# Kernel optimization log

Hardware: AMD Instinct MI355X
Metric: run time of the kernel (lower is better)

## Reference

```python
import jax, jax.numpy as jnp
import numpy as np

# ---- static dims ----
B, L, V = 8, 512, 100000
E, NERD, COREFD = 100, 20, 20          # word / ner / coref embedding dims
H, DIS, REL, HT = 128, 20, 97, 512     # hidden, dis embed, relations, n_pairs
W, N, R, C = 512, 32, 8, 256           # DNC word len, cells, read heads, ctrl hidden
IN_SIZE = E + NERD + COREFD            # 140 == H + 12 (required by final_layer)
DNC_OUT = H + 12                        # 140
CTRL_IN = IN_SIZE + R * W               # 4236
MASK_MIN, EPS, CLIP = 0.1, 1e-6, 20.0
# interface vector layout: read keys, read strengths, write key, write strength,
# erase, write vec, free gates, alloc gate, write gate, read modes,
# write mask, read masks, fwd sharpness, bwd sharpness
XI_SIZES = [R*W, R, W, 1, W, W, R, 1, 1, 3*R, W, R*W, R, R]
XI = sum(XI_SIZES)


def setup_inputs():
    key = jax.random.key(0)
    ks = iter(jax.random.split(key, 40))
    def nrm(shape, s=0.02):
        return (jax.random.normal(next(ks), shape) * s).astype(jnp.float32)
    def ri(shape, hi):
        return jax.random.randint(next(ks), shape, 0, hi)
    return dict(
        context_idxs=ri((B, L), V),
        pos=ri((B, L), L),
        context_ner=ri((B, L), 7),
        context_char_idxs=ri((B, L, 16), 262),
        context_lens=jnp.full((B,), L, dtype=jnp.int32),
        h_mapping=jax.random.uniform(next(ks), (B, HT, L), jnp.float32) / L,
        t_mapping=jax.random.uniform(next(ks), (B, HT, L), jnp.float32) / L,
        relation_mask=jnp.ones((B, HT), jnp.float32),
        dis_h_2_t=ri((B, HT), 20),
        dis_t_2_h=ri((B, HT), 20),
        word_emb=nrm((V, E), 0.1),
        entity_emb=nrm((L, COREFD), 0.1),
        ner_emb=nrm((7, NERD), 0.1),
        dis_emb=nrm((20, DIS), 0.1),
        Wih0=nrm((CTRL_IN, 4*C)), Whh0=nrm((C, 4*C)), b0=jnp.zeros((4*C,), jnp.float32),
        Wih1=nrm((C, 4*C)), Whh1=nrm((C, 4*C)), b1=jnp.zeros((4*C,), jnp.float32),
        Wih2=nrm((C, 4*C)), Whh2=nrm((C, 4*C)), b2=jnp.zeros((4*C,), jnp.float32),
        W_xi=nrm((C, XI)), b_xi=jnp.zeros((XI,), jnp.float32),
        W_out=nrm((C + R*W, DNC_OUT)), b_out=jnp.zeros((DNC_OUT,), jnp.float32),
        W_final=nrm((DNC_OUT, 2*H)), b_final=jnp.zeros((2*H,), jnp.float32),
        W_re=nrm((2*H, H)), b_re=jnp.zeros((H,), jnp.float32),
        W_bili=nrm((REL, H+DIS, H+DIS)), b_bili=jnp.zeros((REL,), jnp.float32),
    )


def _lstm(x, h, c, Wih, Whh, b):
    z = x @ Wih + h @ Whh + b
    i, f, g, o = jnp.split(z, 4, axis=-1)
    c = jax.nn.sigmoid(f) * c + jax.nn.sigmoid(i) * jnp.tanh(g)
    h = jax.nn.sigmoid(o) * jnp.tanh(c)
    return h, c


def _content(M, key_, beta, mask):
    # M [B,N,W]; key_, mask [B,h,W]; beta [B,h] -> weights [B,h,N]
    k = key_ * mask
    Mm = M[:, None] * mask[:, :, None]                 # [B,h,N,W]
    dot = jnp.einsum('bhw,bhnw->bhn', k, Mm)
    kn = jnp.linalg.norm(k, axis=-1)[..., None]
    Mn = jnp.linalg.norm(Mm, axis=-1)
    cos = dot / (kn * Mn + EPS)
    return jax.nn.softmax(beta[..., None] * cos, axis=-1)


def _sharpen(w, s):
    w = (w + EPS) ** s[..., None]
    return w / w.sum(-1, keepdims=True)


def _dnc(x, params):
    (Wih0, Whh0, b0, Wih1, Whh1, b1, Wih2, Whh2, b2, W_xi, b_xi, W_out, b_out) = params
    Bs = x.shape[0]
    eye = jnp.eye(N, dtype=x.dtype)
    splits = np.cumsum(XI_SIZES)[:-1]

    def step(carry, x_t):
        (h0, c0, h1, c1, h2, c2, M, u, wr, ww, p, Lnk, reads) = carry
        ci = jnp.concatenate([x_t, reads.reshape(Bs, R*W)], -1)
        h0, c0 = _lstm(ci, h0, c0, Wih0, Whh0, b0)
        h1, c1 = _lstm(h0, h1, c1, Wih1, Whh1, b1)
        h2, c2 = _lstm(h1, h2, c2, Wih2, Whh2, b2)
        h = jnp.clip(h2, -CLIP, CLIP)
        xi = h @ W_xi + b_xi
        (rk, rb, wk, wb, er, wv, fg, ga, gw, rm,
         wmask, rmask, sf, sb) = jnp.split(xi, splits, axis=-1)
        rk = rk.reshape(Bs, R, W)
        rb = 1 + jax.nn.softplus(rb)                    # [B,R]
        wk = wk.reshape(Bs, 1, W)
        wb = 1 + jax.nn.softplus(wb)                    # [B,1]
        er = jax.nn.sigmoid(er)                         # [B,W]
        fg = jax.nn.sigmoid(fg)                         # [B,R]
        ga = jax.nn.sigmoid(ga)
        gw = jax.nn.sigmoid(gw)
        pi = jax.nn.softmax(rm.reshape(Bs, R, 3), -1)
        wmask = MASK_MIN + (1 - MASK_MIN) * jax.nn.sigmoid(wmask)
        rmask = MASK_MIN + (1 - MASK_MIN) * jax.nn.sigmoid(rmask).reshape(Bs, R, W)
        sf = 1 + jax.nn.softplus(sf)
        sb = 1 + jax.nn.softplus(sb)

        # retention / usage
        psi = jnp.prod(1 - fg[:, :, None] * wr, axis=1)  # [B,N]
        u = (u + ww - u * ww) * psi
        # allocation weighting via sorted free list
        order = jnp.argsort(u, axis=-1)
        us = jnp.take_along_axis(u, order, -1)
        cp = jnp.cumprod(jnp.concatenate([jnp.ones((Bs, 1), u.dtype), us[:, :-1]], -1), -1)
        a_s = (1 - us) * cp
        a = jnp.zeros_like(u).at[jnp.arange(Bs)[:, None], order].set(a_s)
        # write addressing (masked content + allocation)
        cw = _content(M, wk, wb, wmask[:, None, :])[:, 0]
        ww = gw * (ga * a + (1 - ga) * cw)
        # de-allocate content of freed cells, then write
        M = M * psi[:, :, None]
        M = M * (1 - ww[:, :, None] * er[:, None, :]) + ww[:, :, None] * wv[:, None, :]
        # temporal link matrix (uses previous precedence p)
        Lnk = (1 - ww[:, :, None] - ww[:, None, :]) * Lnk + ww[:, :, None] * p[:, None, :]
        Lnk = Lnk * (1 - eye)
        p = (1 - ww.sum(-1, keepdims=True)) * p + ww
        # read addressing with link sharpness control
        fw = _sharpen(jnp.einsum('bij,brj->bri', Lnk, wr), sf)
        bw = _sharpen(jnp.einsum('bji,brj->bri', Lnk, wr), sb)
        cr = _content(M, rk, rb, rmask)
        wr = pi[..., 0:1] * bw + pi[..., 1:2] * cr + pi[..., 2:3] * fw
        reads = jnp.einsum('brn,bnw->brw', wr, M)
        y = jnp.concatenate([h, reads.reshape(Bs, R*W)], -1) @ W_out + b_out
        return (h0, c0, h1, c1, h2, c2, M, u, wr, ww, p, Lnk, reads), y

    z = jnp.zeros
    carry0 = (z((Bs, C)), z((Bs, C)), z((Bs, C)), z((Bs, C)), z((Bs, C)), z((Bs, C)),
              z((Bs, N, W)), z((Bs, N)), z((Bs, R, N)), z((Bs, N)), z((Bs, N)),
              z((Bs, N, N)), z((Bs, R, W)))
    _, ys = jax.lax.scan(step, carry0, x.transpose(1, 0, 2))
    return ys.transpose(1, 0, 2)  # [B,L,DNC_OUT]


def reference(context_idxs, pos, context_ner, context_char_idxs, context_lens,
              h_mapping, t_mapping, relation_mask, dis_h_2_t, dis_t_2_h,
              word_emb, entity_emb, ner_emb, dis_emb,
              Wih0, Whh0, b0, Wih1, Whh1, b1, Wih2, Whh2, b2,
              W_xi, b_xi, W_out, b_out, W_final, b_final, W_re, b_re,
              W_bili, b_bili):
    sent = jnp.concatenate([word_emb[context_idxs], entity_emb[pos],
                            ner_emb[context_ner]], -1)      # [B,L,140]
    dnc_params = (Wih0, Whh0, b0, Wih1, Whh1, b1, Wih2, Whh2, b2,
                  W_xi, b_xi, W_out, b_out)
    out = _dnc(sent, dnc_params)                             # [B,L,140]
    out = out @ W_final + b_final                            # LockedDropout: identity (eval)
    ctx = jax.nn.relu(out @ W_re + b_re)                     # [B,L,H]
    s0 = jnp.einsum('bpl,blh->bph', h_mapping, ctx)
    t0 = jnp.einsum('bpl,blh->bph', t_mapping, ctx)
    s_rep = jnp.concatenate([s0, dis_emb[dis_h_2_t]], -1)    # [B,P,148]
    t_rep = jnp.concatenate([t0, dis_emb[dis_t_2_h]], -1)
    return jnp.einsum('bpi,kij,bpj->bpk', s_rep, W_bili, t_rep) + b_bili
```

## Files before the change

### kernel.cpp

```cpp
#include <hip/hip_runtime.h>
#include <math.h>

#define B8      8
#define LSEQ    512
#define NWG     256
#define TPB     512
#define RELK    97
#define BI      148
#define FSTR    16

#define oWA     0
#define oW1     18432
#define oW2     20480
#define oWX     22528
#define oWY     34816
#define oST     37196
#define LDSF    40948
#define LDSB    (LDSF*4)

__device__ __forceinline__ float sigf(float x){
  return (x >= 0.f) ? 1.f/(1.f + expf(-x)) : expf(x)/(1.f + expf(x));
}
__device__ __forceinline__ float spf(float x){
  return (x > 0.f) ? x + log1pf(expf(-x)) : log1pf(expf(x));
}
__device__ __forceinline__ float agld(const float* p){
  return __hip_atomic_load(p, __ATOMIC_RELAXED, __HIP_MEMORY_SCOPE_AGENT);
}
__device__ __forceinline__ void agst(float* p, float v){
  __hip_atomic_store(p, v, __ATOMIC_RELAXED, __HIP_MEMORY_SCOPE_AGENT);
}

__global__ __launch_bounds__(256)
void k_sent(const int* __restrict__ cidx, const int* __restrict__ pos,
            const int* __restrict__ ner, const float* __restrict__ wemb,
            const float* __restrict__ eemb, const float* __restrict__ nemb,
            float* __restrict__ sent)
{
  int flat = blockIdx.x*256 + threadIdx.x;
  if (flat >= B8*LSEQ*140) return;
  int d = flat % 140; int bl = flat / 140;
  float v;
  if (d < 100)      v = wemb[(size_t)cidx[bl]*100 + d];
  else if (d < 120) v = eemb[(size_t)pos[bl]*20 + (d-100)];
  else              v = nemb[(size_t)ner[bl]*20 + (d-120)];
  sent[flat] = v;
}

__global__ __launch_bounds__(256)
void k_tr(const float* __restrict__ A, const float* __restrict__ Bsrc,
          int N, int K1a, int K1b, int K2, long long total, float* __restrict__ T)
{
  long long i = (long long)blockIdx.x*256 + threadIdx.x;
  if (i >= total) return;
  int k = (int)(i % K2);
  long long c = i / K2;
  float v = 0.f;
  if (k < K1a)            v = A[(size_t)k*N + c];
  else if (k < K1a+K1b)   v = Bsrc[(size_t)(k-K1a)*N + c];
  T[i] = v;
}

__device__ __forceinline__ void gbar(int* flags, int* genrep, int seq){
  __syncthreads();
  const int tid = threadIdx.x;
  const int bid = blockIdx.x;
  if (tid == 0){
    asm volatile("s_waitcnt vmcnt(0)" ::: "memory");
    __hip_atomic_store(&flags[bid*FSTR], seq, __ATOMIC_RELAXED, __HIP_MEMORY_SCOPE_AGENT);
  }
  if (bid == 0){
    if (tid < NWG){
      while (__hip_atomic_load(&flags[tid*FSTR], __ATOMIC_RELAXED, __HIP_MEMORY_SCOPE_AGENT) < seq)
        __builtin_amdgcn_s_sleep(1);
    }
    __syncthreads();
    if (tid < NWG)
      __hip_atomic_store(&genrep[tid*FSTR], seq, __ATOMIC_RELAXED, __HIP_MEMORY_SCOPE_AGENT);
  } else if (tid == 0){
    while (__hip_atomic_load(&genrep[bid*FSTR], __ATOMIC_RELAXED, __HIP_MEMORY_SCOPE_AGENT) < seq)
      __builtin_amdgcn_s_sleep(1);
  }
  __syncthreads();
}

__device__ void mem_phase(float* lds, const float* __restrict__ xi,
                          float* __restrict__ M, float* u_g, float* ww_g,
                          float* p_g, float* wr_g, float* L_g, float* rout)
{
  const int tid = threadIdx.x;
  float* mL  = lds;
  float* mwr = lds+1024;
  float* mwrn= lds+1280;
  float* mcr = lds+1536;
  float* mfw = lds+1792;
  float* mbw = lds+2048;
  float* PSI = lds+2304;
  float* UU  = lds+2336;
  float* US  = lds+2368;
  float* AA  = lds+2400;
  float* CW  = lds+2432;
  float* WWN = lds+2464;
  float* WWO = lds+2496;
  float* PP  = lds+2528;
  int*   mord= (int*)(lds+2560);
  float* mh  = lds+2592;
  float* mpi = lds+2624;
  float* msc = lds+2648;
  float* q1  = lds+2688;
  float* q2  = lds+3200;

  if (tid < 8){
    mh[tid]    = 1.f + spf(agld(&xi[4096+tid]));
    mh[8+tid]  = 1.f + spf(agld(&xi[10283+tid]));
    mh[16+tid] = 1.f + spf(agld(&xi[10291+tid]));
    mh[24+tid] = sigf(agld(&xi[5641+tid]));
    float e0=agld(&xi[5651+3*tid]), e1=agld(&xi[5652+3*tid]), e2=agld(&xi[5653+3*tid]);
    float mx=fmaxf(e0,fmaxf(e1,e2));
    float x0=expf(e0-mx), x1=expf(e1-mx), x2=expf(e2-mx);
    float inv=1.f/(x0+x1+x2);
    mpi[tid*3]=x0*inv; mpi[tid*3+1]=x1*inv; mpi[tid*3+2]=x2*inv;
  }
  if (tid==0){ msc[0]=1.f+spf(agld(&xi[4616])); msc[1]=sigf(agld(&xi[5649])); msc[2]=sigf(agld(&xi[5650])); }
  if (tid<32){ UU[tid]=u_g[tid]; WWO[tid]=ww_g[tid]; PP[tid]=p_g[tid]; }
  if (tid<256) mwr[tid]=wr_g[tid];
  mL[tid]=L_g[tid]; mL[tid+512]=L_g[tid+512];
  { float wm = 0.1f+0.9f*sigf(agld(&xi[5675+tid])); q1[tid]=agld(&xi[4104+tid])*wm; q2[tid]=wm; }
  __syncthreads();

  if (tid<32){
    float psi=1.f;
    #pragma unroll
    for (int r=0;r<8;r++) psi *= (1.f - mh[24+r]*mwr[r*32+tid]);
    PSI[tid]=psi;
    float uo=UU[tid], wo=WWO[tid];
    UU[tid]=(uo+wo-uo*wo)*psi;
  }
  __syncthreads();
  if (tid<32){
    float un=UU[tid]; int rank=0;
    for (int m=0;m<32;m++){ float um=UU[m]; rank += (um<un)||(um==un && m<tid); }
    mord[rank]=tid;
  }
  __syncthreads();
  if (tid<32) US[tid]=UU[mord[tid]];
  __syncthreads();
  if (tid==0){ float cp=1.f; for (int j=0;j<32;j++){ AA[mord[j]]=(1.f-US[j])*cp; cp*=US[j]; } }
  __syncthreads();

  { float q=q1[tid]*q1[tid];
    for (int o=32;o;o>>=1) q += __shfl_down(q,o,64);
    if ((tid&63)==0) msc[8+(tid>>6)]=q; }
  __syncthreads();
  if (tid==0){ float q=0.f; for (int i=0;i<8;i++) q+=msc[8+i]; msc[3]=sqrtf(q); }
  __syncthreads();
  { int n=tid>>4, wsub=tid&15;
    float d=0.f,q=0.f;
    for (int i=0;i<32;i++){ int w=wsub+16*i; float m=M[(size_t)n*512+w]; float t2=m*q2[w]; d+=q1[w]*t2; q+=t2*t2; }
    for (int o=8;o;o>>=1){ d+=__shfl_down(d,o,16); q+=__shfl_down(q,o,16); }
    if (wsub==0){ float cs=d/(msc[3]*sqrtf(q)+1e-6f); CW[n]=msc[0]*cs; } }
  __syncthreads();
  if (tid==0){ float mx=-1e30f; for(int n=0;n<32;n++) mx=fmaxf(mx,CW[n]); msc[4]=mx; }
  __syncthreads();
  if (tid<32) CW[tid]=expf(CW[tid]-msc[4]);
  __syncthreads();
  if (tid==0){ float sm=0.f; for(int n=0;n<32;n++) sm+=CW[n]; msc[5]=1.f/sm; }
  __syncthreads();
  if (tid<32) CW[tid]*=msc[5];
  __syncthreads();
  if (tid<32) WWN[tid]=msc[2]*(msc[1]*AA[tid]+(1.f-msc[1])*CW[tid]);
  __syncthreads();
  { float er=sigf(agld(&xi[4617+tid])); float wv=agld(&xi[5129+tid]);
    for (int n=0;n<32;n++){ size_t idx=(size_t)n*512+tid; float m=M[idx];
      M[idx]=m*PSI[n]*(1.f-WWN[n]*er)+WWN[n]*wv; } }
  __syncthreads();
  for (int ii=0;ii<2;ii++){ int f=tid+512*ii; int i=f>>5, j=f&31;
    float nl=(1.f-WWN[i]-WWN[j])*mL[f]+WWN[i]*PP[j];
    mL[f]=(i==j)?0.f:nl; }
  __syncthreads();
  if (tid==0){ float sw=0.f; for(int n=0;n<32;n++) sw+=WWN[n]; msc[6]=sw; }
  __syncthreads();
  if (tid<32) PP[tid]=(1.f-msc[6])*PP[tid]+WWN[tid];
  __syncthreads();
  { int r=(tid>>5)&7, i=tid&31; bool isB=(tid>=256);
    float accv=0.f;
    if (!isB){ for (int j=0;j<32;j++) accv += mL[i*32+j]*mwr[r*32+j]; }
    else     { for (int j=0;j<32;j++) accv += mL[j*32+i]*mwr[r*32+j]; }
    float sp = isB? mh[16+r] : mh[8+r];
    float e = expf(sp*logf(accv+1e-6f));
    if (!isB) mfw[r*32+i]=e; else mbw[r*32+i]=e; }
  __syncthreads();
  if (tid<16){ int r=tid&7; float sm=0.f;
    if (tid<8){ for(int n=0;n<32;n++) sm+=mfw[r*32+n]; msc[16+r]=1.f/sm; }
    else      { for(int n=0;n<32;n++) sm+=mbw[r*32+n]; msc[24+r]=1.f/sm; } }
  __syncthreads();
  { int r=(tid>>5)&7, i=tid&31; bool isB=(tid>=256);
    if (!isB) mfw[r*32+i]*=msc[16+r]; else mbw[r*32+i]*=msc[24+r]; }
  __syncthreads();
  for (int r=0;r<8;r++){
    { float rm=0.1f+0.9f*sigf(agld(&xi[6187+r*512+tid]));
      q1[tid]=agld(&xi[r*512+tid])*rm; q2[tid]=rm; }
    __syncthreads();
    { float q=q1[tid]*q1[tid];
      for (int o=32;o;o>>=1) q+=__shfl_down(q,o,64);
      if ((tid&63)==0) msc[8+(tid>>6)]=q; }
    __syncthreads();
    if (tid==0){ float qq=0.f; for(int i=0;i<8;i++) qq+=msc[8+i]; msc[32]=sqrtf(qq); }
    __syncthreads();
    { int n=tid>>4, wsub=tid&15;
      float d=0.f,q=0.f;
      for (int i=0;i<32;i++){ int w=wsub+16*i; float m=M[(size_t)n*512+w]; float t2=m*q2[w]; d+=q1[w]*t2; q+=t2*t2; }
      for (int o=8;o;o>>=1){ d+=__shfl_down(d,o,16); q+=__shfl_down(q,o,16); }
      if (wsub==0){ float cs=d/(msc[32]*sqrtf(q)+1e-6f); mcr[r*32+n]=mh[r]*cs; } }
    __syncthreads();
  }
  if (tid<8){ int r=tid; float mx=-1e30f;
    for (int n=0;n<32;n++) mx=fmaxf(mx,mcr[r*32+n]);
    float sm=0.f;
    for (int n=0;n<32;n++){ float e=expf(mcr[r*32+n]-mx); mcr[r*32+n]=e; sm+=e; }
    float inv=1.f/sm;
    for (int n=0;n<32;n++) mcr[r*32+n]*=inv; }
  __syncthreads();
  if (tid<256){ int r=tid>>5, n=tid&31;
    float v=mpi[r*3]*mbw[r*32+n]+mpi[r*3+1]*mcr[r*32+n]+mpi[r*3+2]*mfw[r*32+n];
    mwrn[tid]=v; wr_g[tid]=v; }
  __syncthreads();
  { int r=tid>>6, wsub=tid&63;
    for (int i2=0;i2<8;i2++){ int w=wsub+64*i2;
      float accv=0.f;
      for (int n=0;n<32;n++) accv+=mwrn[r*32+n]*M[(size_t)n*512+w];
      agst(&rout[r*512+w], accv); } }
  if (tid<32){ u_g[tid]=UU[tid]; ww_g[tid]=WWN[tid]; p_g[tid]=PP[tid]; }
  L_g[tid]=mL[tid]; L_g[tid+512]=mL[tid+512];
}

__global__ __launch_bounds__(TPB, 1)
void dnc_persist(
  const float* __restrict__ sent,
  const float* __restrict__ Wih0, const float* __restrict__ Whh0, const float* __restrict__ b0,
  const float* __restrict__ Wih1, const float* __restrict__ Whh1, const float* __restrict__ b1,
  const float* __restrict__ Wih2, const float* __restrict__ Whh2, const float* __restrict__ b2,
  const float* __restrict__ WXIT, const float* __restrict__ bxi,
  const float* __restrict__ Wout, const float* __restrict__ bout,
  float* __restrict__ yh,
  float* __restrict__ reads,
  float* __restrict__ h0, float* __restrict__ h1,
  float* __restrict__ h2u, float* __restrict__ h2c,
  float* __restrict__ c0p, float* __restrict__ c1p, float* __restrict__ c2p,
  float* __restrict__ zp0, float* __restrict__ zp1, float* __restrict__ zp2,
  float* __restrict__ yp, float* __restrict__ xig,
  float* __restrict__ Mb, float* __restrict__ ug, float* __restrict__ wwg,
  float* __restrict__ pg, float* __restrict__ wrg, float* __restrict__ Lg,
  int* flags, int* genrep)
{
  extern __shared__ float lds[];
  const int wg  = blockIdx.x;
  const int tid = threadIdx.x;
  const int cg  = wg >> 4, kg  = wg & 15;
  const int cgB = wg >> 3, kgB = wg & 7;
  const int ycg = wg >> 6, ykg = wg & 63;
  const int xc  = tid >> 6, xk = tid & 63;
  float* stg = lds + oST;
  int seq = 0;

  for (int f=tid; f<18432; f+=TPB){
    int kk=f>>6, cc=f&63;
    int gk=kg*288+kk, gc=cg*64+cc;
    float v=0.f;
    if (gk<4236) v=Wih0[(size_t)gk*1024+gc];
    else if (gk<4492) v=Whh0[(size_t)(gk-4236)*1024+gc];
    lds[oWA+f]=v;
  }
  for (int f=tid; f<2048; f+=TPB){
    int kk=f>>5, cc=f&31;
    int gk=kgB*64+kk, gc=cgB*32+cc;
    lds[oW1+f] = (gk<256)? Wih1[(size_t)gk*1024+gc] : Whh1[(size_t)(gk-256)*1024+gc];
  }
  for (int f=tid; f<2048; f+=TPB){
    int kk=f>>5, cc=f&31;
    int gk=kgB*64+kk, gc=cgB*32+cc;
    lds[oW2+f] = (gk<256)? Wih2[(size_t)gk*1024+gc] : Whh2[(size_t)(gk-256)*1024+gc];
  }
  for (int f=tid; f<12288; f+=TPB){
    int cl=f>>8, k=f&255; int col=wg*48+cl;
    lds[oWX+f] = (col<10299)? WXIT[(size_t)col*256+k] : 0.f;
  }
  for (int f=tid; f<2380; f+=TPB){
    int kk=f/35, cc=f%35;
    int gk=ykg*68+kk, gc=ycg*35+cc;
    lds[oWY+f] = Wout[(size_t)gk*140+gc];
  }
  __syncthreads();

  #pragma unroll 1
  for (int t=0; t<LSEQ; t++){
    {
      float* sAct = stg;
      float* sActY= stg+2304;
      for (int f=tid; f<2304; f+=TPB){
        int s=f/288, kk=f%288; int g=kg*288+kk;
        float v;
        if (g<140)       v = sent[((size_t)s*512+t)*140+g];
        else if (g<4236) v = agld(&reads[s*4096+g-140]);
        else if (g<4492) v = agld(&h0[s*256+(g-4236)]);
        else             v = 0.f;
        sAct[f]=v;
      }
      if (t>0) for (int f=tid; f<544; f+=TPB){
        int s=f/68, kk=f%68; int gy=ykg*68+kk;
        sActY[f] = (gy<256)? agld(&h2c[s*256+gy]) : agld(&reads[s*4096+gy-256]);
      }
      __syncthreads();
      { int cc=tid&63, s=tid>>6;
        const float* wAl = lds+oWA;
        const float* ac  = sAct + s*288;
        float acc=0.f;
        #pragma unroll 8
        for (int kk=0; kk<288; kk++) acc += wAl[kk*64+cc]*ac[kk];
        agst(&zp0[(size_t)(kg*8+s)*1024 + cg*64+cc], acc); }
      if (t>0 && tid<280){ int s=tid/35, cc=tid%35;
        const float* wYl = lds+oWY;
        const float* ac  = sActY + s*68;
        float acc=0.f;
        #pragma unroll 4
        for (int kk=0; kk<68; kk++) acc += wYl[kk*35+cc]*ac[kk];
        agst(&yp[(size_t)(ykg*8+s)*144 + ycg*35+cc], acc); }
    }
    gbar(flags,genrep,++seq);

    if (wg < 64){
      int s = wg>>3, part = wg&7;
      float* sP = stg;
      { int j32=tid&31, q=(tid>>5)&3, kp=tid>>7;
        int col = q*256 + part*32 + j32;
        float v=0.f;
        for (int k2=kp*4; k2<kp*4+4; k2++) v += agld(&zp0[(size_t)(k2*8+s)*1024+col]);
        sP[kp*128 + q*32 + j32] = v; }
      __syncthreads();
      if (tid<32){
        int j = part*32 + tid;
        float zq[4];
        #pragma unroll
        for (int q=0;q<4;q++){ float v=0.f;
          for (int k2=0;k2<4;k2++) v += sP[k2*128+q*32+tid];
          zq[q]=v + b0[q*256+j]; }
        float cold=c0p[s*256+j];
        float cn=sigf(zq[1])*cold + sigf(zq[0])*tanhf(zq[2]);
        float h=sigf(zq[3])*tanhf(cn);
        c0p[s*256+j]=cn;
        agst(&h0[s*256+j], h);
      }
    }
    gbar(flags,genrep,++seq);

    {
      float* sAct = stg;
      for (int f=tid; f<512; f+=TPB){ int s=f>>6, kk=f&63; int g=kgB*64+kk;
        sAct[f] = (g<256)? agld(&h0[s*256+g]) : agld(&h1[s*256+g-256]); }
      __syncthreads();
      if (tid<256){ int cc=tid&31, s=tid>>5;
        const float* w1l = lds+oW1;
        const float* ac  = sAct + s*64;
        float acc=0.f;
        #pragma unroll 8
        for (int kk=0; kk<64; kk++) acc += w1l[kk*32+cc]*ac[kk];
        agst(&zp1[(size_t)(kgB*8+s)*1024 + cgB*32+cc], acc); }
    }
    gbar(flags,genrep,++seq);

    if (wg < 64){
      int s = wg>>3, part = wg&7;
      float* sP = stg;
      if (tid<256){ int j32=tid&31, q=(tid>>5)&3, kp=tid>>7;
        int col = q*256 + part*32 + j32;
        float v=0.f;
        for (int k2=kp*4; k2<kp*4+4; k2++) v += agld(&zp1[(size_t)(k2*8+s)*1024+col]);
        sP[kp*128 + q*32 + j32] = v; }
      __syncthreads();
      if (tid<32){
        int j = part*32 + tid;
        float zq[4];
        #pragma unroll
        for (int q=0;q<4;q++) zq[q]=sP[q*32+tid]+sP[128+q*32+tid]+b1[q*256+j];
        float cold=c1p[s*256+j];
        float cn=sigf(zq[1])*cold + sigf(zq[0])*tanhf(zq[2]);
        float h=sigf(zq[3])*tanhf(cn);
        c1p[s*256+j]=cn;
        agst(&h1[s*256+j], h);
      }
    }
    gbar(flags,genrep,++seq);

    {
      float* sAct = stg;
      for (int f=tid; f<512; f+=TPB){ int s=f>>6, kk=f&63; int g=kgB*64+kk;
        sAct[f] = (g<256)? agld(&h1[s*256+g]) : agld(&h2u[s*256+g-256]); }
      __syncthreads();
      if (tid<256){ int cc=tid&31, s=tid>>5;
        const float* w2l = lds+oW2;
        const float* ac  = sAct + s*64;
        float acc=0.f;
        #pragma unroll 8
        for (int kk=0; kk<64; kk++) acc += w2l[kk*32+cc]*ac[kk];
        agst(&zp2[(size_t)(kgB*8+s)*1024 + cgB*32+cc], acc); }
    }
    gbar(flags,genrep,++seq);

    if (wg < 64){
      int s = wg>>3, part = wg&7;
      float* sP = stg;
      if (tid<256){ int j32=tid&31, q=(tid>>5)&3, kp=tid>>7;
        int col = q*256 + part*32 + j32;
        float v=0.f;
        for (int k2=kp*4; k2<kp*4+4; k2++) v += agld(&zp2[(size_t)(k2*8+s)*1024+col]);
        sP[kp*128 + q*32 + j32] = v; }
      __syncthreads();
      if (tid<32){
        int j = part*32 + tid;
        float zq[4];
        #pragma unroll
        for (int q=0;q<4;q++) zq[q]=sP[q*32+tid]+sP[128+q*32+tid]+b2[q*256+j];
        float cold=c2p[s*256+j];
        float cn=sigf(zq[1])*cold + sigf(zq[0])*tanhf(zq[2]);
        float h2=sigf(zq[3])*tanhf(cn);
        float hc=fminf(fmaxf(h2,-20.f),20.f);
        c2p[s*256+j]=cn;
        agst(&h2u[s*256+j], h2);
        agst(&h2c[s*256+j], hc);
      }
    }
    gbar(flags,genrep,++seq);

    {
      float* sA2 = stg;
      for (int f=tid; f<2048; f+=TPB){ int s=f>>8, j=f&255;
        sA2[s*260+j] = agld(&h2c[s*256+j]); }
      __syncthreads();
      float accx[6][8];
      #pragma unroll
      for (int cc=0;cc<6;cc++)
        #pragma unroll
        for (int s=0;s<8;s++) accx[cc][s]=0.f;
      #pragma unroll
      for (int s=0;s<8;s++){
        float4 a = *reinterpret_cast<const float4*>(&sA2[s*260 + (xk<<2)]);
        #pragma unroll
        for (int cc=0;cc<6;cc++){
          float4 wv = *reinterpret_cast<const float4*>(&lds[oWX + (xc*6+cc)*256 + (xk<<2)]);
          accx[cc][s] += a.x*wv.x + a.y*wv.y + a.z*wv.z + a.w*wv.w;
        }
      }
      #pragma unroll
      for (int o=32;o;o>>=1)
        #pragma unroll
        for (int cc=0;cc<6;cc++)
          #pragma unroll
          for (int s=0;s<8;s++) accx[cc][s]+=__shfl_down(accx[cc][s],o,64);
      if ((tid&63)==0){
        #pragma unroll
        for (int cc=0;cc<6;cc++){
          int col = wg*48 + xc*6 + cc;
          if (col < 10299){
            #pragma unroll
            for (int s=0;s<8;s++) agst(&xig[(size_t)s*10299+col], accx[cc][s]+bxi[col]);
          }
        }
      }
    }
    gbar(flags,genrep,++seq);

    if (wg < 8){
      mem_phase(stg, xig + (size_t)wg*10299, Mb + (size_t)wg*16384,
                ug+wg*32, wwg+wg*32, pg+wg*32, wrg+wg*256, Lg+wg*1024,
                reads + wg*4096);
    } else if (wg < 148 && t > 0){
      int ty = t-1, j = wg-8;
      int s = tid>>6, kg2 = tid&63;
      float v = agld(&yp[(size_t)(kg2*8+s)*144 + j]);
      #pragma unroll
      for (int o=32;o;o>>=1) v += __shfl_down(v,o,64);
      if (kg2==0) yh[((size_t)s*512+ty)*140+j] = v + bout[j];
    }
    gbar(flags,genrep,++seq);
  }

  {
    float* sActY = stg;
    for (int f=tid; f<544; f+=TPB){
      int s=f/68, kk=f%68; int gy=ykg*68+kk;
      sActY[f] = (gy<256)? agld(&h2c[s*256+gy]) : agld(&reads[s*4096+gy-256]);
    }
    __syncthreads();
    if (tid<280){ int s=tid/35, cc=tid%35;
      const float* wYl = lds+oWY;
      const float* ac  = sActY + s*68;
      float acc=0.f;
      for (int kk=0; kk<68; kk++) acc += wYl[kk*35+cc]*ac[kk];
      agst(&yp[(size_t)(ykg*8+s)*144 + ycg*35+cc], acc); }
  }
  gbar(flags,genrep,++seq);
  if (wg>=8 && wg<148){
    int j = wg-8;
    int s = tid>>6, kg2 = tid&63;
    float v = agld(&yp[(size_t)(kg2*8+s)*144 + j]);
    #pragma unroll
    for (int o=32;o;o>>=1) v += __shfl_down(v,o,64);
    if (kg2==0) yh[((size_t)s*512+511)*140+j] = v + bout[j];
  }
}

__global__ __launch_bounds__(256)
void gemm16(int M, int N, int K,
            const float* __restrict__ A, long long sAb, int lda,
            const float* __restrict__ Bm, long long sBb, int ldb,
            float* __restrict__ C, long long sCb, int ldc,
            const float* __restrict__ bias, int relu)
{
  __shared__ float sAh[16*512];
  const int tid = threadIdx.x;
  const float* Ab = A + (size_t)blockIdx.y*sAb;
  const float* Bb = Bm + (size_t)blockIdx.y*sBb;
  float* Cb = C + (size_t)blockIdx.y*sCb;
  const int m0 = blockIdx.x*16;
  const int tot = 16*K;
  for (int f = tid; f < tot; f += 256) sAh[f] = Ab[(size_t)m0*lda + f];
  __syncthreads();
  int c = (tid & 63)*4; int rg = tid >> 6;
  if (c >= N) return;
  float acc[4][4] = {};
  for (int k=0;k<K;k++){
    float4 bv = *reinterpret_cast<const float4*>(Bb + (size_t)k*ldb + c);
    #pragma unroll
    for (int rr=0;rr<4;rr++){
      float a = sAh[(rg*4+rr)*K + k];
      acc[rr][0] += a*bv.x; acc[rr][1] += a*bv.y; acc[rr][2] += a*bv.z; acc[rr][3] += a*bv.w;
    }
  }
  for (int rr=0;rr<4;rr++){
    int m = m0 + rg*4 + rr;
    #pragma unroll
    for (int e=0;e<4;e++){
      float v = acc[rr][e] + (bias ? bias[c+e] : 0.f);
      if (relu) v = fmaxf(v, 0.f);
      Cb[(size_t)m*ldc + c + e] = v;
    }
  }
}

__global__ __launch_bounds__(256)
void bilin(const float* __restrict__ s0, const float* __restrict__ t0,
           const float* __restrict__ dis_emb, const int* __restrict__ dht,
           const int* __restrict__ dth, const float* __restrict__ Wb,
           const float* __restrict__ bb, float* __restrict__ out)
{
  __shared__ float sS[BI][33];
  __shared__ float sT[32][152];
  const int tid = threadIdx.x;
  const int bp0 = blockIdx.x*32;
  for (int f = tid; f < 32*BI; f += 256){
    int pp = f / BI, i = f % BI;
    int bp = bp0 + pp;
    float sv, tv;
    if (i < 128){ sv = s0[(size_t)bp*128 + i]; tv = t0[(size_t)bp*128 + i]; }
    else {
      sv = dis_emb[(size_t)dht[bp]*20 + (i-128)];
      tv = dis_emb[(size_t)dth[bp]*20 + (i-128)];
    }
    sS[i][pp] = sv; sT[pp][i] = tv;
  }
  __syncthreads();
  const int ppg = tid >> 5, jb = tid & 31;
  const int pp0 = ppg*4;
  const int k0 = blockIdx.y*49, kend = min(k0+49, RELK);
  for (int k = k0; k < kend; k++){
    const float* Wk = Wb + (size_t)k*BI*BI;
    float acc[4][5];
    #pragma unroll
    for (int a=0;a<4;a++) for (int b=0;b<5;b++) acc[a][b]=0.f;
    for (int i=0;i<BI;i++){
      float sv0 = sS[i][pp0], sv1 = sS[i][pp0+1], sv2 = sS[i][pp0+2], sv3 = sS[i][pp0+3];
      const float* wrow = Wk + i*BI;
      #pragma unroll
      for (int jj=0;jj<5;jj++){
        int j = jb + 32*jj;
        if (j < BI){
          float w = wrow[j];
          acc[0][jj] += sv0*w; acc[1][jj] += sv1*w; acc[2][jj] += sv2*w; acc[3][jj] += sv3*w;
        }
      }
    }
    float dot[4] = {0.f,0.f,0.f,0.f};
    #pragma unroll
    for (int jj=0;jj<5;jj++){
      int j = jb + 32*jj;
      if (j < BI){
        #pragma unroll
        for (int p4=0;p4<4;p4++) dot[p4] += acc[p4][jj]*sT[pp0+p4][j];
      }
    }
    #pragma unroll
    for (int p4=0;p4<4;p4++)
      for (int o=16;o;o>>=1) dot[p4] += __shfl_down(dot[p4], o, 32);
    if (jb == 0){
      #pragma unroll
      for (int p4=0;p4<4;p4++)
        out[(size_t)(bp0+pp0+p4)*RELK + k] = dot[p4] + bb[k];
    }
  }
}

extern "C" void kernel_launch(void* const* d_in, const int* in_sizes, int n_in,
                              void* d_out, int out_size, void* d_ws, size_t ws_size,
                              hipStream_t stream)
{
  (void)in_sizes; (void)n_in; (void)out_size; (void)ws_size;
  const int*   ctx_idx = (const int*)  d_in[0];
  const int*   pos     = (const int*)  d_in[1];
  const int*   nerI    = (const int*)  d_in[2];
  const float* h_map   = (const float*)d_in[5];
  const float* t_map   = (const float*)d_in[6];
  const int*   dht     = (const int*)  d_in[8];
  const int*   dth     = (const int*)  d_in[9];
  const float* wemb    = (const float*)d_in[10];
  const float* eemb    = (const float*)d_in[11];
  const float* nemb    = (const float*)d_in[12];
  const float* demb    = (const float*)d_in[13];
  const float* Wih0    = (const float*)d_in[14];
  const float* Whh0    = (const float*)d_in[15];
  const float* b0      = (const float*)d_in[16];
  const float* Wih1    = (const float*)d_in[17];
  const float* Whh1    = (const float*)d_in[18];
  const float* b1      = (const float*)d_in[19];
  const float* Wih2    = (const float*)d_in[20];
  const float* Whh2    = (const float*)d_in[21];
  const float* b2      = (const float*)d_in[22];
  const float* Wxi     = (const float*)d_in[23];
  const float* bxi     = (const float*)d_in[24];
  const float* Wout    = (const float*)d_in[25];
  const float* bout    = (const float*)d_in[26];
  const float* Wfin    = (const float*)d_in[27];
  const float* bfin    = (const float*)d_in[28];
  const float* Wre     = (const float*)d_in[29];
  const float* bre     = (const float*)d_in[30];
  const float* Wbili   = (const float*)d_in[31];
  const float* bbili   = (const float*)d_in[32];

  float* ws    = (float*)d_ws;
  float* sent  = ws;
  float* yh    = sent + 573440;
  float* o256  = yh + 573440;
  float* s0b   = o256 + 1048576;
  float* t0b   = s0b + 524288;
  float* SB    = t0b + 524288;
  float* reads = SB + 0;
  float* h0    = SB + 32768;
  float* h1    = SB + 34816;
  float* h2u   = SB + 36864;
  float* h2c   = SB + 38912;
  float* c0p   = SB + 40960;
  float* c1p   = SB + 43008;
  float* c2p   = SB + 45056;
  float* zp0   = SB + 47104;
  float* zp1   = SB + 178176;
  float* zp2   = SB + 243712;
  float* yp    = SB + 309248;
  float* xig   = SB + 382976;
  float* Mb    = SB + 465368;
  float* ug    = SB + 596440;
  float* wwg   = SB + 596696;
  float* pg    = SB + 596952;
  float* wrg   = SB + 597208;
  float* Lg    = SB + 599256;
  float* barf  = SB + 607448;
  float* SEnd  = SB + 615640;
  float* WXIT  = SEnd;
  float* ctxb  = yh;
  int* flags  = (int*)barf;
  int* genrep = flags + 256*FSTR;

  hipMemsetAsync(SB, 0, (size_t)615640*sizeof(float), stream);

  hipLaunchKernelGGL(k_tr, dim3(10299), dim3(256), 0, stream,
                     Wxi, Wxi, 10299, 256, 0, 256, (long long)2636544, WXIT);
  hipLaunchKernelGGL(k_sent, dim3((573440+255)/256), dim3(256), 0, stream,
                     ctx_idx, pos, nerI, wemb, eemb, nemb, sent);

  hipFuncSetAttribute(reinterpret_cast<const void*>(dnc_persist),
                      hipFuncAttributeMaxDynamicSharedMemorySize, LDSB);

  hipLaunchKernelGGL(dnc_persist, dim3(NWG), dim3(TPB), LDSB, stream,
                     sent, Wih0, Whh0, b0, Wih1, Whh1, b1, Wih2, Whh2, b2,
                     WXIT, bxi, Wout, bout, yh, reads,
                     h0, h1, h2u, h2c, c0p, c1p, c2p,
                     zp0, zp1, zp2, yp, xig,
                     Mb, ug, wwg, pg, wrg, Lg, flags, genrep);

  hipLaunchKernelGGL(gemm16, dim3(256,1), dim3(256), 0, stream,
                     4096, 256, 140, yh, (long long)0, 140, Wfin, (long long)0, 256,
                     o256, (long long)0, 256, bfin, 0);
  hipLaunchKernelGGL(gemm16, dim3(256,1), dim3(256), 0, stream,
                     4096, 128, 256, o256, (long long)0, 256, Wre, (long long)0, 128,
                     ctxb, (long long)0, 128, bre, 1);
  hipLaunchKernelGGL(gemm16, dim3(32,8), dim3(256), 0, stream,
                     512, 128, 512, h_map, (long long)(512*512), 512,
                     ctxb, (long long)(512*128), 128,
                     s0b, (long long)(512*128), 128, (const float*)nullptr, 0);
  hipLaunchKernelGGL(gemm16, dim3(32,8), dim3(256), 0, stream,
                     512, 128, 512, t_map, (long long)(512*512), 512,
                     ctxb, (long long)(512*128), 128,
                     t0b, (long long)(512*128), 128, (const float*)nullptr, 0);
  hipLaunchKernelGGL(bilin, dim3(128,2), dim3(256), 0, stream,
                     s0b, t0b, demb, dht, dth, Wbili, bbili, (float*)d_out);
}
```

Measured before the change: 90.09 ms.

## Use counter-based grid barrier and 64-bit vectorized atomics in persistent DNC kernel

New measurement: 99.87 ms. 10.9% more time.

```diff
diff --git a/kernel.cpp b/kernel.cpp
--- a/kernel.cpp
+++ b/kernel.cpp
@@ -8,6 +8,7 @@
 #define RELK    97
 #define BI      148
 #define FSTR    16
+#define XIP     10312
 
 #define oWA     0
 #define oW1     18432
@@ -29,6 +30,22 @@
 }
 __device__ __forceinline__ void agst(float* p, float v){
   __hip_atomic_store(p, v, __ATOMIC_RELAXED, __HIP_MEMORY_SCOPE_AGENT);
+}
+__device__ __forceinline__ float2 agld2(const float* p){
+  union{ unsigned long long u; float2 f; } c;
+  c.u = __hip_atomic_load((const unsigned long long*)p, __ATOMIC_RELAXED, __HIP_MEMORY_SCOPE_AGENT);
+  return c.f;
+}
+__device__ __forceinline__ void agst2(float* p, float2 v){
+  union{ unsigned long long u; float2 f; } c; c.f = v;
+  __hip_atomic_store((unsigned long long*)p, c.u, __ATOMIC_RELAXED, __HIP_MEMORY_SCOPE_AGENT);
+}
+__device__ __forceinline__ int ximap(int c){
+  if (c < 4617)  return c;
+  if (c < 5641)  return c+3;
+  if (c < 5650)  return c+3;
+  if (c < 5651)  return c+6;
+  return c+9;
 }
 
 __global__ __launch_bounds__(256)
@@ -61,25 +78,19 @@
   T[i] = v;
 }
 
-__device__ __forceinline__ void gbar(int* flags, int* genrep, int seq){
-  __syncthreads();
-  const int tid = threadIdx.x;
-  const int bid = blockIdx.x;
-  if (tid == 0){
+__device__ __forceinline__ void gbar(int* cnt, int* genrep, int seq){
+  __syncthreads();
+  if (threadIdx.x == 0){
     asm volatile("s_waitcnt vmcnt(0)" ::: "memory");
-    __hip_atomic_store(&flags[bid*FSTR], seq, __ATOMIC_RELAXED, __HIP_MEMORY_SCOPE_AGENT);
-  }
-  if (bid == 0){
-    if (tid < NWG){
-      while (__hip_atomic_load(&flags[tid*FSTR], __ATOMIC_RELAXED, __HIP_MEMORY_SCOPE_AGENT) < seq)
+    int prev = __hip_atomic_fetch_add(cnt, 1, __ATOMIC_ACQ_REL, __HIP_MEMORY_SCOPE_AGENT);
+    if (prev == seq*NWG - 1){
+      #pragma unroll
+      for (int i=0;i<32;i++)
+        __hip_atomic_store(&genrep[i*FSTR], seq, __ATOMIC_RELAXED, __HIP_MEMORY_SCOPE_AGENT);
+    } else {
+      while (__hip_atomic_load(&genrep[(blockIdx.x & 31)*FSTR], __ATOMIC_RELAXED, __HIP_MEMORY_SCOPE_AGENT) < seq)
         __builtin_amdgcn_s_sleep(1);
     }
-    __syncthreads();
-    if (tid < NWG)
-      __hip_atomic_store(&genrep[tid*FSTR], seq, __ATOMIC_RELAXED, __HIP_MEMORY_SCOPE_AGENT);
-  } else if (tid == 0){
-    while (__hip_atomic_load(&genrep[bid*FSTR], __ATOMIC_RELAXED, __HIP_MEMORY_SCOPE_AGENT) < seq)
-      __builtin_amdgcn_s_sleep(1);
   }
   __syncthreads();
 }
@@ -109,23 +120,31 @@
   float* msc = lds+2648;
   float* q1  = lds+2688;
   float* q2  = lds+3200;
+  float* q1b = lds;
+  float* q2b = lds+512;
 
   if (tid < 8){
     mh[tid]    = 1.f + spf(agld(&xi[4096+tid]));
-    mh[8+tid]  = 1.f + spf(agld(&xi[10283+tid]));
-    mh[16+tid] = 1.f + spf(agld(&xi[10291+tid]));
-    mh[24+tid] = sigf(agld(&xi[5641+tid]));
-    float e0=agld(&xi[5651+3*tid]), e1=agld(&xi[5652+3*tid]), e2=agld(&xi[5653+3*tid]);
+    mh[8+tid]  = 1.f + spf(agld(&xi[10292+tid]));
+    mh[16+tid] = 1.f + spf(agld(&xi[10300+tid]));
+    mh[24+tid] = sigf(agld(&xi[5644+tid]));
+    float e0=agld(&xi[5660+3*tid]), e1=agld(&xi[5661+3*tid]), e2=agld(&xi[5662+3*tid]);
     float mx=fmaxf(e0,fmaxf(e1,e2));
     float x0=expf(e0-mx), x1=expf(e1-mx), x2=expf(e2-mx);
     float inv=1.f/(x0+x1+x2);
     mpi[tid*3]=x0*inv; mpi[tid*3+1]=x1*inv; mpi[tid*3+2]=x2*inv;
   }
-  if (tid==0){ msc[0]=1.f+spf(agld(&xi[4616])); msc[1]=sigf(agld(&xi[5649])); msc[2]=sigf(agld(&xi[5650])); }
+  if (tid==0){ msc[0]=1.f+spf(agld(&xi[4616])); msc[1]=sigf(agld(&xi[5652])); msc[2]=sigf(agld(&xi[5656])); }
   if (tid<32){ UU[tid]=u_g[tid]; WWO[tid]=ww_g[tid]; PP[tid]=p_g[tid]; }
   if (tid<256) mwr[tid]=wr_g[tid];
   mL[tid]=L_g[tid]; mL[tid+512]=L_g[tid+512];
-  { float wm = 0.1f+0.9f*sigf(agld(&xi[5675+tid])); q1[tid]=agld(&xi[4104+tid])*wm; q2[tid]=wm; }
+  if (tid<256){
+    float2 wmv=agld2(&xi[5684+2*tid]);
+    float2 wkv=agld2(&xi[4104+2*tid]);
+    float wm0=0.1f+0.9f*sigf(wmv.x), wm1=0.1f+0.9f*sigf(wmv.y);
+    q1[2*tid]=wkv.x*wm0; q1[2*tid+1]=wkv.y*wm1;
+    q2[2*tid]=wm0;       q2[2*tid+1]=wm1;
+  }
   __syncthreads();
 
   if (tid<32){
@@ -170,9 +189,17 @@
   __syncthreads();
   if (tid<32) WWN[tid]=msc[2]*(msc[1]*AA[tid]+(1.f-msc[1])*CW[tid]);
   __syncthreads();
-  { float er=sigf(agld(&xi[4617+tid])); float wv=agld(&xi[5129+tid]);
-    for (int n=0;n<32;n++){ size_t idx=(size_t)n*512+tid; float m=M[idx];
-      M[idx]=m*PSI[n]*(1.f-WWN[n]*er)+WWN[n]*wv; } }
+  if (tid<256){
+    float2 erv=agld2(&xi[4620+2*tid]);
+    float2 wvv=agld2(&xi[5132+2*tid]);
+    float er0=sigf(erv.x), er1=sigf(erv.y);
+    for (int n=0;n<32;n++){
+      float2 m = *(const float2*)&M[(size_t)n*512+2*tid];
+      m.x = m.x*PSI[n]*(1.f-WWN[n]*er0) + WWN[n]*wvv.x;
+      m.y = m.y*PSI[n]*(1.f-WWN[n]*er1) + WWN[n]*wvv.y;
+      *(float2*)&M[(size_t)n*512+2*tid] = m;
+    }
+  }
   __syncthreads();
   for (int ii=0;ii<2;ii++){ int f=tid+512*ii; int i=f>>5, j=f&31;
     float nl=(1.f-WWN[i]-WWN[j])*mL[f]+WWN[i]*PP[j];
@@ -197,21 +224,44 @@
   { int r=(tid>>5)&7, i=tid&31; bool isB=(tid>=256);
     if (!isB) mfw[r*32+i]*=msc[16+r]; else mbw[r*32+i]*=msc[24+r]; }
   __syncthreads();
-  for (int r=0;r<8;r++){
-    { float rm=0.1f+0.9f*sigf(agld(&xi[6187+r*512+tid]));
-      q1[tid]=agld(&xi[r*512+tid])*rm; q2[tid]=rm; }
+  L_g[tid]=mL[tid]; L_g[tid+512]=mL[tid+512];
+  __syncthreads();
+  for (int hp=0; hp<4; hp++){
+    if (tid<256){
+      #pragma unroll
+      for (int rp=0;rp<2;rp++){
+        int r=2*hp+rp;
+        float* tq1 = rp? q1b : q1;
+        float* tq2 = rp? q2b : q2;
+        float2 rmv=agld2(&xi[6196+r*512+2*tid]);
+        float2 rkv=agld2(&xi[(size_t)r*512+2*tid]);
+        float rm0=0.1f+0.9f*sigf(rmv.x), rm1=0.1f+0.9f*sigf(rmv.y);
+        tq1[2*tid]=rkv.x*rm0; tq1[2*tid+1]=rkv.y*rm1;
+        tq2[2*tid]=rm0;       tq2[2*tid+1]=rm1;
+      }
+    }
     __syncthreads();
-    { float q=q1[tid]*q1[tid];
+    { int rp=tid>>8, w2=tid&255;
+      const float* tq1 = rp? q1b : q1;
+      float a=tq1[2*w2], b=tq1[2*w2+1];
+      float q=a*a+b*b;
       for (int o=32;o;o>>=1) q+=__shfl_down(q,o,64);
       if ((tid&63)==0) msc[8+(tid>>6)]=q; }
     __syncthreads();
-    if (tid==0){ float qq=0.f; for(int i=0;i<8;i++) qq+=msc[8+i]; msc[32]=sqrtf(qq); }
+    if (tid<2){ float qq=0.f; for (int i=0;i<4;i++) qq+=msc[8+tid*4+i]; msc[32+tid]=sqrtf(qq); }
     __syncthreads();
-    { int n=tid>>4, wsub=tid&15;
+    { int rp=tid>>8, rem=tid&255, n=rem>>3, wsub=rem&7;
+      const float* tq1 = rp? q1b : q1;
+      const float* tq2 = rp? q2b : q2;
       float d=0.f,q=0.f;
-      for (int i=0;i<32;i++){ int w=wsub+16*i; float m=M[(size_t)n*512+w]; float t2=m*q2[w]; d+=q1[w]*t2; q+=t2*t2; }
-      for (int o=8;o;o>>=1){ d+=__shfl_down(d,o,16); q+=__shfl_down(q,o,16); }
-      if (wsub==0){ float cs=d/(msc[32]*sqrtf(q)+1e-6f); mcr[r*32+n]=mh[r]*cs; } }
+      for (int i3=0;i3<32;i3++){ int w=wsub*64+2*i3;
+        float2 m = *(const float2*)&M[(size_t)n*512+w];
+        float t0=m.x*tq2[w], t1=m.y*tq2[w+1];
+        d += tq1[w]*t0 + tq1[w+1]*t1;
+        q += t0*t0 + t1*t1;
+      }
+      for (int o=4;o;o>>=1){ d+=__shfl_down(d,o,8); q+=__shfl_down(q,o,8); }
+      if (wsub==0){ int r=2*hp+rp; float cs=d/(msc[32+rp]*sqrtf(q)+1e-6f); mcr[r*32+n]=mh[r]*cs; } }
     __syncthreads();
   }
   if (tid<8){ int r=tid; float mx=-1e30f;
@@ -226,12 +276,13 @@
     mwrn[tid]=v; wr_g[tid]=v; }
   __syncthreads();
   { int r=tid>>6, wsub=tid&63;
-    for (int i2=0;i2<8;i2++){ int w=wsub+64*i2;
-      float accv=0.f;
-      for (int n=0;n<32;n++) accv+=mwrn[r*32+n]*M[(size_t)n*512+w];
-      agst(&rout[r*512+w], accv); } }
+    for (int i3=0;i3<4;i3++){ int w=wsub*8+2*i3;
+      float2 acc=make_float2(0.f,0.f);
+      for (int n=0;n<32;n++){ float wr=mwrn[r*32+n];
+        float2 m = *(const float2*)&M[(size_t)n*512+w];
+        acc.x+=wr*m.x; acc.y+=wr*m.y; }
+      agst2(&rout[r*512+w], acc); } }
   if (tid<32){ u_g[tid]=UU[tid]; ww_g[tid]=WWN[tid]; p_g[tid]=PP[tid]; }
-  L_g[tid]=mL[tid]; L_g[tid+512]=mL[tid+512];
 }
 
 __global__ __launch_bounds__(TPB, 1)
@@ -251,7 +302,7 @@
   float* __restrict__ yp, float* __restrict__ xig,
   float* __restrict__ Mb, float* __restrict__ ug, float* __restrict__ wwg,
   float* __restrict__ pg, float* __restrict__ wrg, float* __restrict__ Lg,
-  int* flags, int* genrep)
+  int* cnt, int* genrep)
 {
   extern __shared__ float lds[];
   const int wg  = blockIdx.x;
@@ -297,18 +348,19 @@
     {
       float* sAct = stg;
       float* sActY= stg+2304;
-      for (int f=tid; f<2304; f+=TPB){
-        int s=f/288, kk=f%288; int g=kg*288+kk;
-        float v;
-        if (g<140)       v = sent[((size_t)s*512+t)*140+g];
-        else if (g<4236) v = agld(&reads[s*4096+g-140]);
-        else if (g<4492) v = agld(&h0[s*256+(g-4236)]);
-        else             v = 0.f;
-        sAct[f]=v;
-      }
-      if (t>0) for (int f=tid; f<544; f+=TPB){
-        int s=f/68, kk=f%68; int gy=ykg*68+kk;
-        sActY[f] = (gy<256)? agld(&h2c[s*256+gy]) : agld(&reads[s*4096+gy-256]);
+      for (int f2=tid; f2<1152; f2+=TPB){
+        int s=f2/144, kk=(f2%144)*2; int g=kg*288+kk;
+        float2 v;
+        if (g<140)       v = *(const float2*)&sent[((size_t)s*512+t)*140+g];
+        else if (g<4236) v = agld2(&reads[s*4096+g-140]);
+        else if (g<4492) v = agld2(&h0[s*256+(g-4236)]);
+        else             v = make_float2(0.f,0.f);
+        *(float2*)&sAct[s*288+kk] = v;
+      }
+      if (t>0) for (int f2=tid; f2<272; f2+=TPB){
+        int s=f2/34, kk=(f2%34)*2; int gy=ykg*68+kk;
+        float2 v = (gy<256)? agld2(&h2c[s*256+gy]) : agld2(&reads[s*4096+gy-256]);
+        *(float2*)&sActY[s*68+kk] = v;
       }
       __syncthreads();
       { int cc=tid&63, s=tid>>6;
@@ -317,7 +369,9 @@
         float acc=0.f;
         #pragma unroll 8
         for (int kk=0; kk<288; kk++) acc += wAl[kk*64+cc]*ac[kk];
-        agst(&zp0[(size_t)(kg*8+s)*1024 + cg*64+cc], acc); }
+        float accO = __shfl_xor(acc, 1, 64);
+        if (!(tid&1))
+          agst2(&zp0[(size_t)(kg*8+s)*1024 + cg*64+cc], make_float2(acc,accO)); }
       if (t>0 && tid<280){ int s=tid/35, cc=tid%35;
         const float* wYl = lds+oWY;
         const float* ac  = sActY + s*68;
@@ -326,37 +380,43 @@
         for (int kk=0; kk<68; kk++) acc += wYl[kk*35+cc]*ac[kk];
         agst(&yp[(size_t)(ykg*8+s)*144 + ycg*35+cc], acc); }
     }
-    gbar(flags,genrep,++seq);
+    gbar(cnt,genrep,++seq);
 
     if (wg < 64){
       int s = wg>>3, part = wg&7;
       float* sP = stg;
-      { int j32=tid&31, q=(tid>>5)&3, kp=tid>>7;
-        int col = q*256 + part*32 + j32;
-        float v=0.f;
-        for (int k2=kp*4; k2<kp*4+4; k2++) v += agld(&zp0[(size_t)(k2*8+s)*1024+col]);
-        sP[kp*128 + q*32 + j32] = v; }
+      { int j2=tid&15, q=(tid>>4)&3, kp=tid>>6;
+        int col = q*256 + part*32 + j2*2;
+        float2 v = make_float2(0.f,0.f);
+        for (int k2=kp*2; k2<kp*2+2; k2++){
+          float2 a = agld2(&zp0[(size_t)(k2*8+s)*1024+col]);
+          v.x+=a.x; v.y+=a.y; }
+        sP[kp*128 + q*32 + j2*2]   = v.x;
+        sP[kp*128 + q*32 + j2*2+1] = v.y; }
       __syncthreads();
       if (tid<32){
         int j = part*32 + tid;
         float zq[4];
         #pragma unroll
         for (int q=0;q<4;q++){ float v=0.f;
-          for (int k2=0;k2<4;k2++) v += sP[k2*128+q*32+tid];
+          for (int kp=0;kp<8;kp++) v += sP[kp*128+q*32+tid];
           zq[q]=v + b0[q*256+j]; }
         float cold=c0p[s*256+j];
         float cn=sigf(zq[1])*cold + sigf(zq[0])*tanhf(zq[2]);
         float h=sigf(zq[3])*tanhf(cn);
         c0p[s*256+j]=cn;
-        agst(&h0[s*256+j], h);
-      }
-    }
-    gbar(flags,genrep,++seq);
+        float hO=__shfl_xor(h,1,64);
+        if (!(tid&1)) agst2(&h0[s*256+j], make_float2(h,hO));
+      }
+    }
+    gbar(cnt,genrep,++seq);
 
     {
       float* sAct = stg;
-      for (int f=tid; f<512; f+=TPB){ int s=f>>6, kk=f&63; int g=kgB*64+kk;
-        sAct[f] = (g<256)? agld(&h0[s*256+g]) : agld(&h1[s*256+g-256]); }
+      for (int f2=tid; f2<256; f2+=TPB){
+        int s=f2>>5, kk=(f2&31)*2; int g=kgB*64+kk;
+        float2 v = (g<256)? agld2(&h0[s*256+g]) : agld2(&h1[s*256+g-256]);
+        *(float2*)&sAct[s*64+kk] = v; }
       __syncthreads();
       if (tid<256){ int cc=tid&31, s=tid>>5;
         const float* w1l = lds+oW1;
@@ -364,37 +424,43 @@
         float acc=0.f;
         #pragma unroll 8
         for (int kk=0; kk<64; kk++) acc += w1l[kk*32+cc]*ac[kk];
-        agst(&zp1[(size_t)(kgB*8+s)*1024 + cgB*32+cc], acc); }
-    }
-    gbar(flags,genrep,++seq);
+        float accO = __shfl_xor(acc, 1, 64);
+        if (!(tid&1))
+          agst2(&zp1[(size_t)(kgB*8+s)*1024 + cgB*32+cc], make_float2(acc,accO)); }
+    }
+    gbar(cnt,genrep,++seq);
 
     if (wg < 64){
       int s = wg>>3, part = wg&7;
       float* sP = stg;
-      if (tid<256){ int j32=tid&31, q=(tid>>5)&3, kp=tid>>7;
-        int col = q*256 + part*32 + j32;
-        float v=0.f;
-        for (int k2=kp*4; k2<kp*4+4; k2++) v += agld(&zp1[(size_t)(k2*8+s)*1024+col]);
-        sP[kp*128 + q*32 + j32] = v; }
+      { int j2=tid&15, q=(tid>>4)&3, kp=tid>>6;
+        float2 a = agld2(&zp1[(size_t)(kp*8+s)*1024 + q*256+part*32+j2*2]);
+        sP[kp*128 + q*32 + j2*2]   = a.x;
+        sP[kp*128 + q*32 + j2*2+1] = a.y; }
       __syncthreads();
       if (tid<32){
         int j = part*32 + tid;
         float zq[4];
         #pragma unroll
-        for (int q=0;q<4;q++) zq[q]=sP[q*32+tid]+sP[128+q*32+tid]+b1[q*256+j];
+        for (int q=0;q<4;q++){ float v=0.f;
+          for (int kp=0;kp<8;kp++) v += sP[kp*128+q*32+tid];
+          zq[q]=v + b1[q*256+j]; }
         float cold=c1p[s*256+j];
         float cn=sigf(zq[1])*cold + sigf(zq[0])*tanhf(zq[2]);
         float h=sigf(zq[3])*tanhf(cn);
         c1p[s*256+j]=cn;
-        agst(&h1[s*256+j], h);
-      }
-    }
-    gbar(flags,genrep,++seq);
+        float hO=__shfl_xor(h,1,64);
+        if (!(tid&1)) agst2(&h1[s*256+j], make_float2(h,hO));
+      }
+    }
+    gbar(cnt,genrep,++seq);
 
     {
       float* sAct = stg;
-      for (int f=tid; f<512; f+=TPB){ int s=f>>6, kk=f&63; int g=kgB*64+kk;
-        sAct[f] = (g<256)? agld(&h1[s*256+g]) : agld(&h2u[s*256+g-256]); }
+      for (int f2=tid; f2<256; f2+=TPB){
+        int s=f2>>5, kk=(f2&31)*2; int g=kgB*64+kk;
+        float2 v = (g<256)? agld2(&h1[s*256+g]) : agld2(&h2u[s*256+g-256]);
+        *(float2*)&sAct[s*64+kk] = v; }
       __syncthreads();
       if (tid<256){ int cc=tid&31, s=tid>>5;
         const float* w2l = lds+oW2;
@@ -402,39 +468,46 @@
         float acc=0.f;
         #pragma unroll 8
         for (int kk=0; kk<64; kk++) acc += w2l[kk*32+cc]*ac[kk];
-        agst(&zp2[(size_t)(kgB*8+s)*1024 + cgB*32+cc], acc); }
-    }
-    gbar(flags,genrep,++seq);
+        float accO = __shfl_xor(acc, 1, 64);
+        if (!(tid&1))
+          agst2(&zp2[(size_t)(kgB*8+s)*1024 + cgB*32+cc], make_float2(acc,accO)); }
+    }
+    gbar(cnt,genrep,++seq);
 
     if (wg < 64){
       int s = wg>>3, part = wg&7;
       float* sP = stg;
-      if (tid<256){ int j32=tid&31, q=(tid>>5)&3, kp=tid>>7;
-        int col = q*256 + part*32 + j32;
-        float v=0.f;
-        for (int k2=kp*4; k2<kp*4+4; k2++) v += agld(&zp2[(size_t)(k2*8+s)*1024+col]);
-        sP[kp*128 + q*32 + j32] = v; }
+      { int j2=tid&15, q=(tid>>4)&3, kp=tid>>6;
+        float2 a = agld2(&zp2[(size_t)(kp*8+s)*1024 + q*256+part*32+j2*2]);
+        sP[kp*128 + q*32 + j2*2]   = a.x;
+        sP[kp*128 + q*32 + j2*2+1] = a.y; }
       __syncthreads();
       if (tid<32){
         int j = part*32 + tid;
         float zq[4];
         #pragma unroll
-        for (int q=0;q<4;q++) zq[q]=sP[q*32+tid]+sP[128+q*32+tid]+b2[q*256+j];
+        for (int q=0;q<4;q++){ float v=0.f;
+          for (int kp=0;kp<8;kp++) v += sP[kp*128+q*32+tid];
+          zq[q]=v + b2[q*256+j]; }
         float cold=c2p[s*256+j];
         float cn=sigf(zq[1])*cold + sigf(zq[0])*tanhf(zq[2]);
         float h2=sigf(zq[3])*tanhf(cn);
         float hc=fminf(fmaxf(h2,-20.f),20.f);
         c2p[s*256+j]=cn;
-        agst(&h2u[s*256+j], h2);
-        agst(&h2c[s*256+j], hc);
-      }
-    }
-    gbar(flags,genrep,++seq);
+        float h2O=__shfl_xor(h2,1,64), hcO=__shfl_xor(hc,1,64);
+        if (!(tid&1)){
+          agst2(&h2u[s*256+j], make_float2(h2,h2O));
+          agst2(&h2c[s*256+j], make_float2(hc,hcO)); }
+      }
+    }
+    gbar(cnt,genrep,++seq);
 
     {
       float* sA2 = stg;
-      for (int f=tid; f<2048; f+=TPB){ int s=f>>8, j=f&255;
-        sA2[s*260+j] = agld(&h2c[s*256+j]); }
+      for (int f2=tid; f2<1024; f2+=TPB){
+        int s=f2>>7, j=(f2&127)*2;
+        float2 v = agld2(&h2c[s*256+j]);
+        *(float2*)&sA2[s*260+j] = v; }
       __syncthreads();
       float accx[6][8];
       #pragma unroll
@@ -461,16 +534,17 @@
         for (int cc=0;cc<6;cc++){
           int col = wg*48 + xc*6 + cc;
           if (col < 10299){
+            int pc = ximap(col);
             #pragma unroll
-            for (int s=0;s<8;s++) agst(&xig[(size_t)s*10299+col], accx[cc][s]+bxi[col]);
+            for (int s=0;s<8;s++) agst(&xig[(size_t)s*XIP+pc], accx[cc][s]+bxi[col]);
           }
         }
       }
     }
-    gbar(flags,genrep,++seq);
+    gbar(cnt,genrep,++seq);
 
     if (wg < 8){
-      mem_phase(stg, xig + (size_t)wg*10299, Mb + (size_t)wg*16384,
+      mem_phase(stg, xig + (size_t)wg*XIP, Mb + (size_t)wg*16384,
                 ug+wg*32, wwg+wg*32, pg+wg*32, wrg+wg*256, Lg+wg*1024,
                 reads + wg*4096);
     } else if (wg < 148 && t > 0){
@@ -481,14 +555,15 @@
       for (int o=32;o;o>>=1) v += __shfl_down(v,o,64);
       if (kg2==0) yh[((size_t)s*512+ty)*140+j] = v + bout[j];
     }
-    gbar(flags,genrep,++seq);
+    gbar(cnt,genrep,++seq);
   }
 
   {
     float* sActY = stg;
-    for (int f=tid; f<544; f+=TPB){
-      int s=f/68, kk=f%68; int gy=ykg*68+kk;
-      sActY[f] = (gy<256)? agld(&h2c[s*256+gy]) : agld(&reads[s*4096+gy-256]);
+    for (int f2=tid; f2<272; f2+=TPB){
+      int s=f2/34, kk=(f2%34)*2; int gy=ykg*68+kk;
+      float2 v = (gy<256)? agld2(&h2c[s*256+gy]) : agld2(&reads[s*4096+gy-256]);
+      *(float2*)&sActY[s*68+kk] = v;
     }
     __syncthreads();
     if (tid<280){ int s=tid/35, cc=tid%35;
@@ -498,7 +573,7 @@
       for (int kk=0; kk<68; kk++) acc += wYl[kk*35+cc]*ac[kk];
       agst(&yp[(size_t)(ykg*8+s)*144 + ycg*35+cc], acc); }
   }
-  gbar(flags,genrep,++seq);
+  gbar(cnt,genrep,++seq);
   if (wg>=8 && wg<148){
     int j = wg-8;
     int s = tid>>6, kg2 = tid&63;
@@ -665,20 +740,20 @@
   float* zp2   = SB + 243712;
   float* yp    = SB + 309248;
   float* xig   = SB + 382976;
-  float* Mb    = SB + 465368;
-  float* ug    = SB + 596440;
-  float* wwg   = SB + 596696;
-  float* pg    = SB + 596952;
-  float* wrg   = SB + 597208;
-  float* Lg    = SB + 599256;
-  float* barf  = SB + 607448;
-  float* SEnd  = SB + 615640;
+  float* Mb    = SB + 465472;
+  float* ug    = SB + 596544;
+  float* wwg   = SB + 596800;
+  float* pg    = SB + 597056;
+  float* wrg   = SB + 597312;
+  float* Lg    = SB + 599360;
+  float* barf  = SB + 607552;
+  float* SEnd  = SB + 608576;
   float* WXIT  = SEnd;
   float* ctxb  = yh;
-  int* flags  = (int*)barf;
-  int* genrep = flags + 256*FSTR;
-
-  hipMemsetAsync(SB, 0, (size_t)615640*sizeof(float), stream);
+  int* cnt    = (int*)barf;
+  int* genrep = cnt + FSTR;
+
+  hipMemsetAsync(SB, 0, (size_t)608576*sizeof(float), stream);
 
   hipLaunchKernelGGL(k_tr, dim3(10299), dim3(256), 0, stream,
                      Wxi, Wxi, 10299, 256, 0, 256, (long long)2636544, WXIT);
@@ -693,7 +768,7 @@
                      WXIT, bxi, Wout, bout, yh, reads,
                      h0, h1, h2u, h2c, c0p, c1p, c2p,
                      zp0, zp1, zp2, yp, xig,
-                     Mb, ug, wwg, pg, wrg, Lg, flags, genrep);
+                     Mb, ug, wwg, pg, wrg, Lg, cnt, genrep);
 
   hipLaunchKernelGGL(gemm16, dim3(256,1), dim3(256), 0, stream,
                      4096, 256, 140, yh, (long long)0, 140, Wfin, (long long)0, 256,
```
